# Performance work log

Hardware: AMD Instinct MI355X
Metric: run time of the kernel (lower is better)

Reference implementation:

```python
import jax, jax.numpy as jnp
import numpy as np

B, IN, H, M = 16384, 512, 512, 4096


def setup_inputs() -> dict:
    key = jax.random.key(0)
    ks = jax.random.split(key, 8)
    s_in = 1.0 / np.sqrt(IN + H)
    return {
        "input_tensor": jax.random.normal(ks[0], (B, IN), jnp.float32),
        "hidden": jax.random.normal(ks[1], (B, H), jnp.float32),
        "cell": jax.random.normal(ks[2], (B, H), jnp.float32),
        # fused gate weights: columns = [input, forget, cell, output] gates
        "W_gates": jax.random.normal(ks[3], (IN + H, 4 * H), jnp.float32) * s_in,
        "b_gates": jnp.zeros((4 * H,), jnp.float32),
        "W_attn": jax.random.normal(ks[4], (H, M), jnp.float32) / np.sqrt(H),
        "b_attn": jnp.zeros((M,), jnp.float32),
        "memory_matrix": jax.random.normal(ks[5], (M, H), jnp.float32) * np.sqrt(2.0 / (M + H)),
    }


def reference(input_tensor, hidden, cell, W_gates, b_gates, W_attn, b_attn, memory_matrix):
    combined = jnp.concatenate([input_tensor, hidden], axis=1)        # (B, IN+H)
    gates = combined @ W_gates + b_gates                              # (B, 4H)
    i_g, f_g, c_g, o_g = jnp.split(gates, 4, axis=1)
    i_g = jax.nn.sigmoid(i_g)
    f_g = jax.nn.sigmoid(f_g)
    c_g = jnp.tanh(c_g)
    o_g = jax.nn.sigmoid(o_g)
    attn = jax.nn.softmax(hidden @ W_attn + b_attn, axis=1)           # (B, M)
    memory_read = attn @ memory_matrix                                # (B, H)
    new_cell = f_g * cell + i_g * c_g + 0.1 * memory_read
    new_hidden = o_g * jnp.tanh(new_cell)
    return (new_hidden, new_cell, attn)
```

## Files before the change

### kernel.cpp

```cpp
#include <hip/hip_runtime.h>
#include <hip/hip_bf16.h>
#include <math.h>

typedef __bf16 bf16_t;
typedef bf16_t bf16x8 __attribute__((ext_vector_type(8)));
typedef float  f32x4  __attribute__((ext_vector_type(4)));

static constexpr int Bn = 16384;
static constexpr int Hn = 512;

__device__ __forceinline__ float sigm(float x) { return 1.0f / (1.0f + __expf(-x)); }

typedef __attribute__((address_space(3))) void lds_void;
typedef const __attribute__((address_space(1))) void gl_void;

__device__ __forceinline__ void glds16(const void* g, void* l) {
    __builtin_amdgcn_global_load_lds((gl_void*)g, (lds_void*)l, 16, 0, 0);
}

__global__ void convert_comb(const float* __restrict__ inp, const float* __restrict__ hid,
                             bf16_t* __restrict__ comb)
{
    size_t t = (size_t)blockIdx.x * blockDim.x + threadIdx.x;
    size_t r = t >> 7;
    int c8 = (int)(t & 127);
    const float* src = (c8 < 64) ? (inp + r * 512 + c8 * 8) : (hid + r * 512 + (c8 - 64) * 8);
    float4 a = ((const float4*)src)[0];
    float4 b = ((const float4*)src)[1];
    bf16x8 o;
    o[0] = (bf16_t)a.x; o[1] = (bf16_t)a.y; o[2] = (bf16_t)a.z; o[3] = (bf16_t)a.w;
    o[4] = (bf16_t)b.x; o[5] = (bf16_t)b.y; o[6] = (bf16_t)b.z; o[7] = (bf16_t)b.w;
    *(bf16x8*)(comb + t * 8) = o;
}

__global__ void transpose_all(const float* __restrict__ Wg, bf16_t* __restrict__ WgT,
                              const float* __restrict__ Wa, bf16_t* __restrict__ WaT,
                              const float* __restrict__ Mem, bf16_t* __restrict__ MemT)
{
    __shared__ float tile[32][33];
    int b = blockIdx.x;
    const float* src; bf16_t* dst; int R, C, gx;
    if (b < 2048)      { src = Wg;  dst = WgT;  R = 1024; C = 2048; gx = 64; }
    else if (b < 4096) { b -= 2048; src = Wa;  dst = WaT;  R = 512;  C = 4096; gx = 128; }
    else               { b -= 4096; src = Mem; dst = MemT; R = 4096; C = 512;  gx = 16; }
    const int x0 = (b % gx) * 32, y0 = (b / gx) * 32;
    const int tx = threadIdx.x & 31, ty = threadIdx.x >> 5;
#pragma unroll
    for (int i = 0; i < 32; i += 8)
        tile[ty + i][tx] = src[(size_t)(y0 + ty + i) * C + x0 + tx];
    __syncthreads();
#pragma unroll
    for (int i = 0; i < 32; i += 8)
        dst[(size_t)(x0 + ty + i) * R + y0 + tx] = (bf16_t)tile[tx][ty + i];
}

template<int EPI>
__global__ __launch_bounds__(512)
void gemm_w8(const bf16_t* __restrict__ A, int lda,
             const bf16_t* __restrict__ Bt, int ldb,
             const float* __restrict__ bias, int K, int N,
             bf16_t* __restrict__ bout, int ost)
{
    __shared__ __align__(16) bf16_t sA[128 * 64];
    __shared__ __align__(16) bf16_t sB[256 * 64];

    const int tid = threadIdx.x, lane = tid & 63, wid = tid >> 6;
    const int wr = wid >> 2, wc = wid & 3;

    const int nwg = gridDim.x;
    int bid = (blockIdx.x & 7) * (nwg >> 3) + (blockIdx.x >> 3);
    const int cbn = N >> 8;
    const int row0 = (bid / cbn) * 128, col0 = (bid % cbn) * 256;

    f32x4 acc[4][4] = {};
    const int nk = K >> 6;
    const int l15 = lane & 15, kq = lane >> 4;

    for (int kt = 0; kt < nk; ++kt) {
        const int k0 = kt << 6;
        {
            const int slot = (lane & 7) ^ (lane >> 3);
#pragma unroll
            for (int t = 0; t < 2; ++t) {
                const int c8 = wid * 2 + t;
                const int r = c8 * 8 + (lane >> 3);
                glds16(A + (size_t)(row0 + r) * lda + k0 + slot * 8, sA + c8 * 512);
            }
#pragma unroll
            for (int t = 0; t < 4; ++t) {
                const int c8 = wid * 4 + t;
                const int r = c8 * 8 + (lane >> 3);
                glds16(Bt + (size_t)(col0 + r) * ldb + k0 + slot * 8, sB + c8 * 512);
            }
        }
        __syncthreads();
#pragma unroll
        for (int ks = 0; ks < 2; ++ks) {
            bf16x8 af[4], bfr[4];
            const int slot = (ks * 4 + kq) ^ (l15 & 7);
#pragma unroll
            for (int j = 0; j < 4; ++j) {
                const int rb = wc * 64 + j * 16 + l15;
                bfr[j] = *(const bf16x8*)&sB[rb * 64 + slot * 8];
                const int ra = wr * 64 + j * 16 + l15;
                af[j] = *(const bf16x8*)&sA[ra * 64 + slot * 8];
            }
#pragma unroll
            for (int i = 0; i < 4; ++i)
#pragma unroll
                for (int j = 0; j < 4; ++j)
                    acc[i][j] = __builtin_amdgcn_mfma_f32_16x16x32_bf16(af[i], bfr[j], acc[i][j], 0, 0, 0);
        }
        __syncthreads();
    }

    const int lr = (lane >> 4) * 4, lc = lane & 15;
#pragma unroll
    for (int i = 0; i < 4; ++i) {
#pragma unroll
        for (int j = 0; j < 4; ++j) {
#pragma unroll
            for (int r = 0; r < 4; ++r) {
                const int grow = row0 + wr * 64 + i * 16 + lr + r;
                const int gcol = col0 + wc * 64 + j * 16 + lc;
                float v = acc[i][j][r] + bias[gcol];
                if constexpr (EPI == 0) {
                    const float a = ((gcol >> 9) == 2) ? tanhf(v) : sigm(v);
                    bout[(size_t)grow * 2048 + gcol] = (bf16_t)a;
                } else {
                    bout[(size_t)grow * ost + gcol] = (bf16_t)__expf(v);
                }
            }
        }
    }
}

__global__ __launch_bounds__(512)
void gemm3o(const bf16_t* __restrict__ E, int estride,
            const bf16_t* __restrict__ MemT,
            const bf16_t* __restrict__ gates, const float* __restrict__ cell,
            float* __restrict__ fout, float* __restrict__ denomBuf)
{
    __shared__ __align__(16) bf16_t sA[64 * 64];
    __shared__ __align__(16) bf16_t sB[256 * 64];

    const int tid = threadIdx.x, lane = tid & 63, wid = tid >> 6;
    const int wr = wid >> 2, wc = wid & 3;

    int bid = (blockIdx.x & 7) * 64 + (blockIdx.x >> 3);
    const int row0 = (bid >> 1) * 64, col0 = (bid & 1) * 256;

    f32x4 acc[2][4] = {};
    f32x4 dacc[2] = {};
    const int l15 = lane & 15, kq = lane >> 4;

    bf16x8 ones;
#pragma unroll
    for (int e = 0; e < 8; ++e) ones[e] = (bf16_t)1.0f;

    for (int kt = 0; kt < 64; ++kt) {
        const int k0 = kt << 6;
        const int slot = (lane & 7) ^ (lane >> 3);
        {
            const int c8 = wid;
            const int r = c8 * 8 + (lane >> 3);
            glds16(E + (size_t)(row0 + r) * estride + k0 + slot * 8, sA + c8 * 512);
        }
#pragma unroll
        for (int t = 0; t < 4; ++t) {
            const int c8 = wid * 4 + t;
            const int r = c8 * 8 + (lane >> 3);
            glds16(MemT + (size_t)(col0 + r) * 4096 + k0 + slot * 8, sB + c8 * 512);
        }
        __syncthreads();
#pragma unroll
        for (int ks = 0; ks < 2; ++ks) {
            bf16x8 af[2], bfr[4];
            const int sl = (ks * 4 + kq) ^ (l15 & 7);
#pragma unroll
            for (int j = 0; j < 4; ++j) {
                const int rb = wc * 64 + j * 16 + l15;
                bfr[j] = *(const bf16x8*)&sB[rb * 64 + sl * 8];
            }
#pragma unroll
            for (int i = 0; i < 2; ++i) {
                const int ra = wr * 32 + i * 16 + l15;
                af[i] = *(const bf16x8*)&sA[ra * 64 + sl * 8];
            }
#pragma unroll
            for (int i = 0; i < 2; ++i) {
#pragma unroll
                for (int j = 0; j < 4; ++j)
                    acc[i][j] = __builtin_amdgcn_mfma_f32_16x16x32_bf16(af[i], bfr[j], acc[i][j], 0, 0, 0);
                dacc[i] = __builtin_amdgcn_mfma_f32_16x16x32_bf16(af[i], ones, dacc[i], 0, 0, 0);
            }
        }
        __syncthreads();
    }

    const int lr = (lane >> 4) * 4, lc = lane & 15;

    if (col0 == 0 && wc == 0 && l15 == 0) {
#pragma unroll
        for (int i = 0; i < 2; ++i)
#pragma unroll
            for (int r = 0; r < 4; ++r)
                denomBuf[row0 + wr * 32 + i * 16 + lr + r] = dacc[i][r];
    }

    float invd[2][4];
#pragma unroll
    for (int i = 0; i < 2; ++i)
#pragma unroll
        for (int r = 0; r < 4; ++r) invd[i][r] = 1.0f / dacc[i][r];

#pragma unroll
    for (int i = 0; i < 2; ++i) {
#pragma unroll
        for (int j = 0; j < 4; ++j) {
#pragma unroll
            for (int r = 0; r < 4; ++r) {
                const int grow = row0 + wr * 32 + i * 16 + lr + r;
                const int gcol = col0 + wc * 64 + j * 16 + lc;
                const float v = acc[i][j][r] * invd[i][r];
                const float ig = (float)gates[(size_t)grow * 2048 + gcol];
                const float fg = (float)gates[(size_t)grow * 2048 + 512 + gcol];
                const float cg = (float)gates[(size_t)grow * 2048 + 1024 + gcol];
                const float og = (float)gates[(size_t)grow * 2048 + 1536 + gcol];
                const float cv = cell[(size_t)grow * 512 + gcol];
                const float ncv = fg * cv + ig * cg + 0.1f * v;
                fout[(size_t)grow * 512 + gcol] = og * tanhf(ncv);
                fout[(size_t)Bn * Hn + (size_t)grow * 512 + gcol] = ncv;
            }
        }
    }
}

__global__ void attn_writer(const bf16_t* __restrict__ E, int estride,
                            const float* __restrict__ denom, float* __restrict__ attn)
{
    const int row = blockIdx.x;
    const bf16_t* lp = E + (size_t)row * estride;
    const float inv = 1.0f / denom[row];
    const int t = threadIdx.x;
    bf16x8 a = ((const bf16x8*)lp)[2 * t];
    bf16x8 b = ((const bf16x8*)lp)[2 * t + 1];
    __syncthreads();
    float* rp = attn + (size_t)row * 4096;
    float4 o0 = { (float)a[0] * inv, (float)a[1] * inv, (float)a[2] * inv, (float)a[3] * inv };
    float4 o1 = { (float)a[4] * inv, (float)a[5] * inv, (float)a[6] * inv, (float)a[7] * inv };
    float4 o2 = { (float)b[0] * inv, (float)b[1] * inv, (float)b[2] * inv, (float)b[3] * inv };
    float4 o3 = { (float)b[4] * inv, (float)b[5] * inv, (float)b[6] * inv, (float)b[7] * inv };
    ((float4*)rp)[4 * t]     = o0;
    ((float4*)rp)[4 * t + 1] = o1;
    ((float4*)rp)[4 * t + 2] = o2;
    ((float4*)rp)[4 * t + 3] = o3;
}

extern "C" void kernel_launch(void* const* d_in, const int* in_sizes, int n_in,
                              void* d_out, int out_size, void* d_ws, size_t ws_size,
                              hipStream_t stream)
{
    const float* input  = (const float*)d_in[0];
    const float* hidden = (const float*)d_in[1];
    const float* cell   = (const float*)d_in[2];
    const float* Wg     = (const float*)d_in[3];
    const float* bg     = (const float*)d_in[4];
    const float* Wa     = (const float*)d_in[5];
    const float* ba     = (const float*)d_in[6];
    const float* Mem    = (const float*)d_in[7];

    float* out  = (float*)d_out;
    float* attn = out + 2ull * Bn * Hn;

    bf16_t* comb  = (bf16_t*)d_ws;
    bf16_t* WgT   = comb + (size_t)Bn * 1024;
    bf16_t* WaT   = WgT + (size_t)2048 * 1024;
    bf16_t* MemT  = WaT + (size_t)4096 * 512;
    bf16_t* gates = MemT + (size_t)512 * 4096;
    float*  denom = (float*)(gates + (size_t)Bn * 2048);
    bf16_t* pws   = (bf16_t*)(denom + Bn);

    const size_t need_big = (size_t)((char*)(pws + (size_t)Bn * 4096) - (char*)d_ws);
    const bool big = ws_size >= need_big;
    bf16_t* Ebuf = big ? pws : (bf16_t*)attn;
    const int estride = big ? 4096 : 8192;

    convert_comb<<<8192, 256, 0, stream>>>(input, hidden, comb);
    transpose_all<<<6144, 256, 0, stream>>>(Wg, WgT, Wa, WaT, Mem, MemT);

    gemm_w8<0><<<1024, 512, 0, stream>>>(comb, 1024, WgT, 1024, bg, 1024, 2048, gates, 2048);
    gemm_w8<1><<<2048, 512, 0, stream>>>(comb + 512, 1024, WaT, 512, ba, 512, 4096,
                                         Ebuf, estride);

    gemm3o<<<512, 512, 0, stream>>>(Ebuf, estride, MemT, gates, cell, out, denom);

    attn_writer<<<Bn, 256, 0, stream>>>(Ebuf, estride, denom, attn);
}
```

Baseline: 425.2 us.

## Merge prologue kernels, enlarge gemm3o row tile, pack two rows per attn_writer block

Merges the bf16 conversion and the weight transposes into one prologue launch. Doubles the gemm3o row tile from 64 to 128, so each block reuses the 256-column MemT tile across twice as many rows, with half as many blocks (256) and double the accumulators. attn_writer now handles two rows per 512-thread block, and the two gate/attention GEMM launches are reordered. The larger tile raises register and LDS pressure and leaves fewer blocks to fill the GPU.

New measurement: 442.4 us. 4.1% more time.

```diff
diff --git a/kernel.cpp b/kernel.cpp
--- a/kernel.cpp
+++ b/kernel.cpp
@@ -18,27 +18,28 @@
     __builtin_amdgcn_global_load_lds((gl_void*)g, (lds_void*)l, 16, 0, 0);
 }
 
-__global__ void convert_comb(const float* __restrict__ inp, const float* __restrict__ hid,
-                             bf16_t* __restrict__ comb)
-{
-    size_t t = (size_t)blockIdx.x * blockDim.x + threadIdx.x;
-    size_t r = t >> 7;
-    int c8 = (int)(t & 127);
-    const float* src = (c8 < 64) ? (inp + r * 512 + c8 * 8) : (hid + r * 512 + (c8 - 64) * 8);
-    float4 a = ((const float4*)src)[0];
-    float4 b = ((const float4*)src)[1];
-    bf16x8 o;
-    o[0] = (bf16_t)a.x; o[1] = (bf16_t)a.y; o[2] = (bf16_t)a.z; o[3] = (bf16_t)a.w;
-    o[4] = (bf16_t)b.x; o[5] = (bf16_t)b.y; o[6] = (bf16_t)b.z; o[7] = (bf16_t)b.w;
-    *(bf16x8*)(comb + t * 8) = o;
-}
-
-__global__ void transpose_all(const float* __restrict__ Wg, bf16_t* __restrict__ WgT,
-                              const float* __restrict__ Wa, bf16_t* __restrict__ WaT,
-                              const float* __restrict__ Mem, bf16_t* __restrict__ MemT)
-{
+__global__ void prologue(const float* __restrict__ inp, const float* __restrict__ hid,
+                         bf16_t* __restrict__ comb,
+                         const float* __restrict__ Wg, bf16_t* __restrict__ WgT,
+                         const float* __restrict__ Wa, bf16_t* __restrict__ WaT,
+                         const float* __restrict__ Mem, bf16_t* __restrict__ MemT)
+{
+    int b = blockIdx.x;
+    if (b < 8192) {
+        size_t t = (size_t)b * blockDim.x + threadIdx.x;
+        size_t r = t >> 7;
+        int c8 = (int)(t & 127);
+        const float* src = (c8 < 64) ? (inp + r * 512 + c8 * 8) : (hid + r * 512 + (c8 - 64) * 8);
+        float4 a = ((const float4*)src)[0];
+        float4 bb = ((const float4*)src)[1];
+        bf16x8 o;
+        o[0] = (bf16_t)a.x; o[1] = (bf16_t)a.y; o[2] = (bf16_t)a.z; o[3] = (bf16_t)a.w;
+        o[4] = (bf16_t)bb.x; o[5] = (bf16_t)bb.y; o[6] = (bf16_t)bb.z; o[7] = (bf16_t)bb.w;
+        *(bf16x8*)(comb + t * 8) = o;
+        return;
+    }
+    b -= 8192;
     __shared__ float tile[32][33];
-    int b = blockIdx.x;
     const float* src; bf16_t* dst; int R, C, gx;
     if (b < 2048)      { src = Wg;  dst = WgT;  R = 1024; C = 2048; gx = 64; }
     else if (b < 4096) { b -= 2048; src = Wa;  dst = WaT;  R = 512;  C = 4096; gx = 128; }
@@ -141,17 +142,17 @@
             const bf16_t* __restrict__ gates, const float* __restrict__ cell,
             float* __restrict__ fout, float* __restrict__ denomBuf)
 {
-    __shared__ __align__(16) bf16_t sA[64 * 64];
+    __shared__ __align__(16) bf16_t sA[128 * 64];
     __shared__ __align__(16) bf16_t sB[256 * 64];
 
     const int tid = threadIdx.x, lane = tid & 63, wid = tid >> 6;
     const int wr = wid >> 2, wc = wid & 3;
 
-    int bid = (blockIdx.x & 7) * 64 + (blockIdx.x >> 3);
-    const int row0 = (bid >> 1) * 64, col0 = (bid & 1) * 256;
-
-    f32x4 acc[2][4] = {};
-    f32x4 dacc[2] = {};
+    int bid = (blockIdx.x & 7) * 32 + (blockIdx.x >> 3);
+    const int row0 = (bid >> 1) * 128, col0 = (bid & 1) * 256;
+
+    f32x4 acc[4][4] = {};
+    f32x4 dacc[4] = {};
     const int l15 = lane & 15, kq = lane >> 4;
 
     bf16x8 ones;
@@ -161,8 +162,9 @@
     for (int kt = 0; kt < 64; ++kt) {
         const int k0 = kt << 6;
         const int slot = (lane & 7) ^ (lane >> 3);
-        {
-            const int c8 = wid;
+#pragma unroll
+        for (int t = 0; t < 2; ++t) {
+            const int c8 = wid * 2 + t;
             const int r = c8 * 8 + (lane >> 3);
             glds16(E + (size_t)(row0 + r) * estride + k0 + slot * 8, sA + c8 * 512);
         }
@@ -175,20 +177,17 @@
         __syncthreads();
 #pragma unroll
         for (int ks = 0; ks < 2; ++ks) {
-            bf16x8 af[2], bfr[4];
+            bf16x8 af[4], bfr[4];
             const int sl = (ks * 4 + kq) ^ (l15 & 7);
 #pragma unroll
             for (int j = 0; j < 4; ++j) {
                 const int rb = wc * 64 + j * 16 + l15;
                 bfr[j] = *(const bf16x8*)&sB[rb * 64 + sl * 8];
-            }
-#pragma unroll
-            for (int i = 0; i < 2; ++i) {
-                const int ra = wr * 32 + i * 16 + l15;
-                af[i] = *(const bf16x8*)&sA[ra * 64 + sl * 8];
-            }
-#pragma unroll
-            for (int i = 0; i < 2; ++i) {
+                const int ra = wr * 64 + j * 16 + l15;
+                af[j] = *(const bf16x8*)&sA[ra * 64 + sl * 8];
+            }
+#pragma unroll
+            for (int i = 0; i < 4; ++i) {
 #pragma unroll
                 for (int j = 0; j < 4; ++j)
                     acc[i][j] = __builtin_amdgcn_mfma_f32_16x16x32_bf16(af[i], bfr[j], acc[i][j], 0, 0, 0);
@@ -202,25 +201,25 @@
 
     if (col0 == 0 && wc == 0 && l15 == 0) {
 #pragma unroll
-        for (int i = 0; i < 2; ++i)
+        for (int i = 0; i < 4; ++i)
 #pragma unroll
             for (int r = 0; r < 4; ++r)
-                denomBuf[row0 + wr * 32 + i * 16 + lr + r] = dacc[i][r];
-    }
-
-    float invd[2][4];
-#pragma unroll
-    for (int i = 0; i < 2; ++i)
+                denomBuf[row0 + wr * 64 + i * 16 + lr + r] = dacc[i][r];
+    }
+
+    float invd[4][4];
+#pragma unroll
+    for (int i = 0; i < 4; ++i)
 #pragma unroll
         for (int r = 0; r < 4; ++r) invd[i][r] = 1.0f / dacc[i][r];
 
 #pragma unroll
-    for (int i = 0; i < 2; ++i) {
+    for (int i = 0; i < 4; ++i) {
 #pragma unroll
         for (int j = 0; j < 4; ++j) {
 #pragma unroll
             for (int r = 0; r < 4; ++r) {
-                const int grow = row0 + wr * 32 + i * 16 + lr + r;
+                const int grow = row0 + wr * 64 + i * 16 + lr + r;
                 const int gcol = col0 + wc * 64 + j * 16 + lc;
                 const float v = acc[i][j][r] * invd[i][r];
                 const float ig = (float)gates[(size_t)grow * 2048 + gcol];
@@ -236,13 +235,14 @@
     }
 }
 
-__global__ void attn_writer(const bf16_t* __restrict__ E, int estride,
-                            const float* __restrict__ denom, float* __restrict__ attn)
-{
-    const int row = blockIdx.x;
+__global__ __launch_bounds__(512)
+void attn_writer(const bf16_t* __restrict__ E, int estride,
+                 const float* __restrict__ denom, float* __restrict__ attn)
+{
+    const int row = blockIdx.x * 2 + (threadIdx.x >> 8);
+    const int t = threadIdx.x & 255;
     const bf16_t* lp = E + (size_t)row * estride;
     const float inv = 1.0f / denom[row];
-    const int t = threadIdx.x;
     bf16x8 a = ((const bf16x8*)lp)[2 * t];
     bf16x8 b = ((const bf16x8*)lp)[2 * t + 1];
     __syncthreads();
@@ -286,14 +286,13 @@
     bf16_t* Ebuf = big ? pws : (bf16_t*)attn;
     const int estride = big ? 4096 : 8192;
 
-    convert_comb<<<8192, 256, 0, stream>>>(input, hidden, comb);
-    transpose_all<<<6144, 256, 0, stream>>>(Wg, WgT, Wa, WaT, Mem, MemT);
-
-    gemm_w8<0><<<1024, 512, 0, stream>>>(comb, 1024, WgT, 1024, bg, 1024, 2048, gates, 2048);
+    prologue<<<14336, 256, 0, stream>>>(input, hidden, comb, Wg, WgT, Wa, WaT, Mem, MemT);
+
     gemm_w8<1><<<2048, 512, 0, stream>>>(comb + 512, 1024, WaT, 512, ba, 512, 4096,
                                          Ebuf, estride);
-
-    gemm3o<<<512, 512, 0, stream>>>(Ebuf, estride, MemT, gates, cell, out, denom);
-
-    attn_writer<<<Bn, 256, 0, stream>>>(Ebuf, estride, denom, attn);
-}
+    gemm_w8<0><<<1024, 512, 0, stream>>>(comb, 1024, WgT, 1024, bg, 1024, 2048, gates, 2048);
+
+    gemm3o<<<256, 512, 0, stream>>>(Ebuf, estride, MemT, gates, cell, out, denom);
+
+    attn_writer<<<8192, 512, 0, stream>>>(Ebuf, estride, denom, attn);
+}
```
